# Performance work log

Hardware: AMD Instinct MI355X
Metric: run time of the kernel (lower is better)

Reference implementation:

```python
import jax, jax.numpy as jnp
import numpy as np

B, N_IN, N_E, N_I, N_OUT, T = 131072, 128, 128, 64, 128, 8


def setup_inputs() -> dict:
    key = jax.random.key(0)
    k0, k1, k2, k3, k4 = jax.random.split(key, 5)
    x = jax.random.normal(k0, (B, N_IN), dtype=jnp.float32)
    # nn.Linear weights are [out_features, in_features]; original init is uniform(0,1).
    # Scale by 1/fan_in to keep the relu recurrence numerically bounded over T steps.
    W_in2E = jax.random.uniform(k1, (N_E, N_IN), dtype=jnp.float32) / N_IN
    W_I2E = jax.random.uniform(k2, (N_E, N_I), dtype=jnp.float32) / N_I
    W_E2I = jax.random.uniform(k3, (N_I, N_E), dtype=jnp.float32) / N_E
    W_E2Out = jax.random.uniform(k4, (N_OUT, N_E), dtype=jnp.float32) / N_E
    return {"x": x, "W_in2E": W_in2E, "W_I2E": W_I2E, "W_E2I": W_E2I,
            "W_E2Out": W_E2Out, "num_timesteps": T}


def reference(x, W_in2E, W_I2E, W_E2I, W_E2Out, num_timesteps):
    # tau = 1 for every population, so each step: state = sum_proj W @ pre_activity,
    # activity = relu(state + bias) with bias = 0 (learn_bias defaults False).
    # Population order within a step: InputE -> H1E -> H1I -> OutE, so H1E uses
    # H1I's activity from the previous step (the recurrent carry).
    ff = x @ W_in2E.T                                  # [B, N_E], constant over steps

    def step(actI, _):
        actE = jax.nn.relu(ff + actI @ W_I2E.T)        # H1.E
        actI_new = jax.nn.relu(actE @ W_E2I.T)         # H1.I (uses current actE)
        out = jax.nn.relu(actE @ W_E2Out.T)            # Output.E
        return actI_new, out

    actI0 = jnp.zeros((x.shape[0], W_I2E.shape[1]), dtype=x.dtype)
    _, outs = jax.lax.scan(step, actI0, None, length=num_timesteps)
    return outs[-1]                                    # output_pop.activity after last step
```

## Files before the change

### kernel.cpp

```cpp
#include <hip/hip_runtime.h>
#include <hip/hip_bf16.h>


typedef __bf16 bf16x8_t __attribute__((ext_vector_type(8)));
typedef __bf16 bf16x4_t __attribute__((ext_vector_type(4)));
typedef float f32x4_t __attribute__((ext_vector_type(4)));

#define THREADS 512

#define S_WIN2E 272
#define S_WE2OUT 272
#define S_WI2E 144
#define S_WE2I 272
#define S_ACTE 272
#define S_ACTI 144

#define OFF_WIN2E 0
#define OFF_WE2OUT (OFF_WIN2E + 128 * S_WIN2E)
#define OFF_WI2E (OFF_WE2OUT + 128 * S_WE2OUT)
#define OFF_WE2I (OFF_WI2E + 128 * S_WI2E)
#define OFF_ACTE (OFF_WE2I + 64 * S_WE2I)
#define OFF_ACTI (OFF_ACTE + 8 * 16 * S_ACTE)
#define SMEM_TOTAL (OFF_ACTI + 8 * 16 * S_ACTI)

__device__ __forceinline__ f32x4_t mfma16(bf16x8_t a, bf16x8_t b, f32x4_t c) {
  return __builtin_amdgcn_mfma_f32_16x16x32_bf16(a, b, c, 0, 0, 0);
}

template <int ROWS, int COLS, int STRIDE_B>
__device__ __forceinline__ void stage_weight(const float* __restrict__ W,
                                             char* dst, int tid) {
  constexpr int TOTAL4 = ROWS * COLS / 4;
#pragma unroll
  for (int it = 0; it < TOTAL4 / THREADS; ++it) {
    int e = (it * THREADS + tid) * 4;
    int r = e / COLS;
    int c = e % COLS;
    float4 v = *reinterpret_cast<const float4*>(W + e);
    bf16x4_t h;
    h[0] = (__bf16)v.x; h[1] = (__bf16)v.y;
    h[2] = (__bf16)v.z; h[3] = (__bf16)v.w;
    *reinterpret_cast<bf16x4_t*>(dst + r * STRIDE_B + c * 2) = h;
  }
}

__global__ __launch_bounds__(THREADS, 2) void unet_fused(
    const float* __restrict__ x,
    const float* __restrict__ Win2E,
    const float* __restrict__ WI2E,
    const float* __restrict__ WE2I,
    const float* __restrict__ WE2Out,
    const int* __restrict__ Tptr,
    float* __restrict__ out) {
  extern __shared__ char smem[];
  const int tid = threadIdx.x;

  stage_weight<128, 128, S_WIN2E>(Win2E, smem + OFF_WIN2E, tid);
  stage_weight<128, 128, S_WE2OUT>(WE2Out, smem + OFF_WE2OUT, tid);
  stage_weight<128, 64, S_WI2E>(WI2E, smem + OFF_WI2E, tid);
  stage_weight<64, 128, S_WE2I>(WE2I, smem + OFF_WE2I, tid);
  __syncthreads();

  const int wid = tid >> 6;
  const int lane = tid & 63;
  const int m = lane & 15;
  const int kc = lane >> 4;
  const int T = *Tptr;

  char* actE = smem + OFF_ACTE + wid * (16 * S_ACTE);
  char* actI = smem + OFF_ACTI + wid * (16 * S_ACTI);

  bf16x8_t wi2e[8][2];
#pragma unroll
  for (int mt = 0; mt < 8; ++mt)
#pragma unroll
    for (int ks = 0; ks < 2; ++ks)
      wi2e[mt][ks] = *reinterpret_cast<const bf16x8_t*>(
          smem + OFF_WI2E + (mt * 16 + m) * S_WI2E + (ks * 32 + kc * 8) * 2);

  bf16x8_t we2i[4][4];
#pragma unroll
  for (int mt = 0; mt < 4; ++mt)
#pragma unroll
    for (int ks = 0; ks < 4; ++ks)
      we2i[mt][ks] = *reinterpret_cast<const bf16x8_t*>(
          smem + OFF_WE2I + (mt * 16 + m) * S_WE2I + (ks * 32 + kc * 8) * 2);

  const long row0 = ((long)blockIdx.x * 8 + wid) * 16;

  bf16x8_t xb[4];
#pragma unroll
  for (int ks = 0; ks < 4; ++ks) {
    const float* xp = x + (row0 + m) * 128 + ks * 32 + kc * 8;
    float4 v0 = *reinterpret_cast<const float4*>(xp);
    float4 v1 = *reinterpret_cast<const float4*>(xp + 4);
    bf16x8_t h;
    h[0] = (__bf16)v0.x; h[1] = (__bf16)v0.y; h[2] = (__bf16)v0.z; h[3] = (__bf16)v0.w;
    h[4] = (__bf16)v1.x; h[5] = (__bf16)v1.y; h[6] = (__bf16)v1.z; h[7] = (__bf16)v1.w;
    xb[ks] = h;
  }

  f32x4_t ff[8];
#pragma unroll
  for (int mt = 0; mt < 8; ++mt) ff[mt] = (f32x4_t){0.f, 0.f, 0.f, 0.f};
#pragma unroll
  for (int ks = 0; ks < 4; ++ks) {
#pragma unroll
    for (int mt = 0; mt < 8; ++mt) {
      bf16x8_t a = *reinterpret_cast<const bf16x8_t*>(
          smem + OFF_WIN2E + (mt * 16 + m) * S_WIN2E + (ks * 32 + kc * 8) * 2);
      ff[mt] = mfma16(a, xb[ks], ff[mt]);
    }
  }

  f32x4_t acc_e[8];
#pragma unroll
  for (int mt = 0; mt < 8; ++mt) acc_e[mt] = ff[mt];

  bf16x8_t eb[4];

  for (int t = 0;; ++t) {
#pragma unroll
    for (int mt = 0; mt < 8; ++mt) {
      bf16x4_t h;
#pragma unroll
      for (int j = 0; j < 4; ++j) h[j] = (__bf16)fmaxf(acc_e[mt][j], 0.f);
      *reinterpret_cast<bf16x4_t*>(actE + m * S_ACTE + (mt * 16 + kc * 4) * 2) = h;
    }
#pragma unroll
    for (int ks = 0; ks < 4; ++ks)
      eb[ks] = *reinterpret_cast<const bf16x8_t*>(
          actE + m * S_ACTE + (ks * 32 + kc * 8) * 2);
    if (t == T - 1) break;

    f32x4_t acc_i[4];
#pragma unroll
    for (int mt = 0; mt < 4; ++mt) acc_i[mt] = (f32x4_t){0.f, 0.f, 0.f, 0.f};
#pragma unroll
    for (int ks = 0; ks < 4; ++ks)
#pragma unroll
      for (int mt = 0; mt < 4; ++mt)
        acc_i[mt] = mfma16(we2i[mt][ks], eb[ks], acc_i[mt]);

#pragma unroll
    for (int mt = 0; mt < 4; ++mt) {
      bf16x4_t h;
#pragma unroll
      for (int j = 0; j < 4; ++j) h[j] = (__bf16)fmaxf(acc_i[mt][j], 0.f);
      *reinterpret_cast<bf16x4_t*>(actI + m * S_ACTI + (mt * 16 + kc * 4) * 2) = h;
    }
    bf16x8_t ib[2];
#pragma unroll
    for (int ks = 0; ks < 2; ++ks)
      ib[ks] = *reinterpret_cast<const bf16x8_t*>(
          actI + m * S_ACTI + (ks * 32 + kc * 8) * 2);

#pragma unroll
    for (int mt = 0; mt < 8; ++mt) acc_e[mt] = ff[mt];
#pragma unroll
    for (int ks = 0; ks < 2; ++ks)
#pragma unroll
      for (int mt = 0; mt < 8; ++mt)
        acc_e[mt] = mfma16(wi2e[mt][ks], ib[ks], acc_e[mt]);
  }

#pragma unroll
  for (int mt = 0; mt < 8; ++mt) {
    f32x4_t o = (f32x4_t){0.f, 0.f, 0.f, 0.f};
#pragma unroll
    for (int ks = 0; ks < 4; ++ks) {
      bf16x8_t a = *reinterpret_cast<const bf16x8_t*>(
          smem + OFF_WE2OUT + (mt * 16 + m) * S_WE2OUT + (ks * 32 + kc * 8) * 2);
      o = mfma16(a, eb[ks], o);
    }
    f32x4_t r;
#pragma unroll
    for (int j = 0; j < 4; ++j) r[j] = fmaxf(o[j], 0.f);
    *reinterpret_cast<f32x4_t*>(out + (row0 + m) * 128 + mt * 16 + kc * 4) = r;
  }
}

extern "C" void kernel_launch(void* const* d_in, const int* in_sizes, int n_in,
                              void* d_out, int out_size, void* d_ws,
                              size_t ws_size, hipStream_t stream) {
  const float* x = (const float*)d_in[0];
  const float* Win2E = (const float*)d_in[1];
  const float* WI2E = (const float*)d_in[2];
  const float* WE2I = (const float*)d_in[3];
  const float* WE2Out = (const float*)d_in[4];
  const int* Tptr = (const int*)d_in[5];
  float* out = (float*)d_out;
  (void)n_in; (void)out_size; (void)d_ws; (void)ws_size;

  const int B = in_sizes[0] / 128;
  (void)hipFuncSetAttribute(reinterpret_cast<const void*>(unet_fused),
                            hipFuncAttributeMaxDynamicSharedMemorySize,
                            SMEM_TOTAL);
  dim3 grid(B / 128), block(THREADS);
  unet_fused<<<grid, block, SMEM_TOTAL, stream>>>(x, Win2E, WI2E, WE2I, WE2Out,
                                                  Tptr, out);
}
```

Baseline: 61.95 us.

## Switch to 32x32 MFMA with register-resident activation transposes via permlane swap

Moves from 16x16x32 to 32x32x16 bf16 MFMA tiles, so each wave now handles 32 batch rows and the grid is halved. Weights are staged into shared memory already in per-lane fragment order, so loads need no padded strides. The per-step activation round trip through shared memory is replaced by in-register relu+pack and v_permlane32_swap to form the next B operands. Weight fragments are now reloaded from LDS on every step instead of being kept in registers, and register pressure from the 16-wide accumulators rises, which may hurt occupancy.

```diff
diff --git a/kernel.cpp b/kernel.cpp
--- a/kernel.cpp
+++ b/kernel.cpp
@@ -3,44 +3,75 @@
 
 
 typedef __bf16 bf16x8_t __attribute__((ext_vector_type(8)));
-typedef __bf16 bf16x4_t __attribute__((ext_vector_type(4)));
+typedef float f32x16_t __attribute__((ext_vector_type(16)));
 typedef float f32x4_t __attribute__((ext_vector_type(4)));
+typedef unsigned int uintx4_t __attribute__((ext_vector_type(4)));
 
 #define THREADS 512
 
-#define S_WIN2E 272
-#define S_WE2OUT 272
-#define S_WI2E 144
-#define S_WE2I 272
-#define S_ACTE 272
-#define S_ACTI 144
+#define OFF_WIN2E 0
+#define OFF_WI2E 32768
+#define OFF_WE2I 49152
+#define OFF_WE2OUT 65536
+#define SMEM_TOTAL 98304
 
-#define OFF_WIN2E 0
-#define OFF_WE2OUT (OFF_WIN2E + 128 * S_WIN2E)
-#define OFF_WI2E (OFF_WE2OUT + 128 * S_WE2OUT)
-#define OFF_WE2I (OFF_WI2E + 128 * S_WI2E)
-#define OFF_ACTE (OFF_WE2I + 64 * S_WE2I)
-#define OFF_ACTI (OFF_ACTE + 8 * 16 * S_ACTE)
-#define SMEM_TOTAL (OFF_ACTI + 8 * 16 * S_ACTI)
-
-__device__ __forceinline__ f32x4_t mfma16(bf16x8_t a, bf16x8_t b, f32x4_t c) {
-  return __builtin_amdgcn_mfma_f32_16x16x32_bf16(a, b, c, 0, 0, 0);
+__device__ __forceinline__ f32x16_t mfma32(bf16x8_t a, bf16x8_t b, f32x16_t c) {
+  return __builtin_amdgcn_mfma_f32_32x32x16_bf16(a, b, c, 0, 0, 0);
 }
 
-template <int ROWS, int COLS, int STRIDE_B>
-__device__ __forceinline__ void stage_weight(const float* __restrict__ W,
-                                             char* dst, int tid) {
-  constexpr int TOTAL4 = ROWS * COLS / 4;
+__device__ __forceinline__ void swap32(unsigned int& x, unsigned int& y) {
+  asm("v_permlane32_swap_b32 %0, %1" : "+v"(x), "+v"(y));
+}
+
+__device__ __forceinline__ unsigned int pack2_relu(float a, float b) {
+  unsigned short lo = __builtin_bit_cast(unsigned short, (__bf16)fmaxf(a, 0.f));
+  unsigned short hi = __builtin_bit_cast(unsigned short, (__bf16)fmaxf(b, 0.f));
+  return (unsigned int)lo | ((unsigned int)hi << 16);
+}
+
+__device__ __forceinline__ void tile_to_bfrags(const f32x16_t& t, bf16x8_t& fa,
+                                               bf16x8_t& fb) {
+  unsigned int P0 = pack2_relu(t[0], t[1]);
+  unsigned int P1 = pack2_relu(t[2], t[3]);
+  unsigned int P2 = pack2_relu(t[4], t[5]);
+  unsigned int P3 = pack2_relu(t[6], t[7]);
+  unsigned int P4 = pack2_relu(t[8], t[9]);
+  unsigned int P5 = pack2_relu(t[10], t[11]);
+  unsigned int P6 = pack2_relu(t[12], t[13]);
+  unsigned int P7 = pack2_relu(t[14], t[15]);
+  swap32(P0, P2);
+  swap32(P1, P3);
+  swap32(P4, P6);
+  swap32(P5, P7);
+  fa = __builtin_bit_cast(bf16x8_t, (uintx4_t){P0, P1, P2, P3});
+  fb = __builtin_bit_cast(bf16x8_t, (uintx4_t){P4, P5, P6, P7});
+}
+
+__device__ __forceinline__ bf16x8_t ldfrag(const char* smem, int off, int fi,
+                                           int lane) {
+  return *reinterpret_cast<const bf16x8_t*>(smem + off + (fi * 64 + lane) * 16);
+}
+
+template <int NMT, int NKS, int COLS>
+__device__ __forceinline__ void stage_frags(const float* __restrict__ W,
+                                            char* dst, int tid) {
+  constexpr int SLOTS = NMT * NKS * 64;
 #pragma unroll
-  for (int it = 0; it < TOTAL4 / THREADS; ++it) {
-    int e = (it * THREADS + tid) * 4;
-    int r = e / COLS;
-    int c = e % COLS;
-    float4 v = *reinterpret_cast<const float4*>(W + e);
-    bf16x4_t h;
-    h[0] = (__bf16)v.x; h[1] = (__bf16)v.y;
-    h[2] = (__bf16)v.z; h[3] = (__bf16)v.w;
-    *reinterpret_cast<bf16x4_t*>(dst + r * STRIDE_B + c * 2) = h;
+  for (int it = 0; it < SLOTS / THREADS; ++it) {
+    int slot = it * THREADS + tid;
+    int lane = slot & 63;
+    int fi = slot >> 6;
+    int mt = fi / NKS, ks = fi % NKS;
+    int cc = lane & 31, hh = lane >> 5;
+    const float* src = W + (mt * 32 + cc) * COLS + ks * 16 + hh * 8;
+    float4 v0 = *reinterpret_cast<const float4*>(src);
+    float4 v1 = *reinterpret_cast<const float4*>(src + 4);
+    bf16x8_t hv;
+    hv[0] = (__bf16)v0.x; hv[1] = (__bf16)v0.y;
+    hv[2] = (__bf16)v0.z; hv[3] = (__bf16)v0.w;
+    hv[4] = (__bf16)v1.x; hv[5] = (__bf16)v1.y;
+    hv[6] = (__bf16)v1.z; hv[7] = (__bf16)v1.w;
+    *reinterpret_cast<bf16x8_t*>(dst + slot * 16) = hv;
   }
 }
 
@@ -55,128 +86,94 @@
   extern __shared__ char smem[];
   const int tid = threadIdx.x;
 
-  stage_weight<128, 128, S_WIN2E>(Win2E, smem + OFF_WIN2E, tid);
-  stage_weight<128, 128, S_WE2OUT>(WE2Out, smem + OFF_WE2OUT, tid);
-  stage_weight<128, 64, S_WI2E>(WI2E, smem + OFF_WI2E, tid);
-  stage_weight<64, 128, S_WE2I>(WE2I, smem + OFF_WE2I, tid);
+  stage_frags<4, 8, 128>(Win2E, smem + OFF_WIN2E, tid);
+  stage_frags<4, 4, 64>(WI2E, smem + OFF_WI2E, tid);
+  stage_frags<2, 8, 128>(WE2I, smem + OFF_WE2I, tid);
+  stage_frags<4, 8, 128>(WE2Out, smem + OFF_WE2OUT, tid);
   __syncthreads();
 
-  const int wid = tid >> 6;
-  const int lane = tid & 63;
-  const int m = lane & 15;
-  const int kc = lane >> 4;
+  const int wid = tid >> 6, lane = tid & 63;
+  const int c = lane & 31, h = lane >> 5;
   const int T = *Tptr;
+  const long row0 = ((long)blockIdx.x * 8 + wid) * 32;
+  const f32x16_t Z = {};
 
-  char* actE = smem + OFF_ACTE + wid * (16 * S_ACTE);
-  char* actI = smem + OFF_ACTI + wid * (16 * S_ACTI);
+  bf16x8_t xb[8];
+#pragma unroll
+  for (int ks = 0; ks < 8; ++ks) {
+    const float* xp = x + (row0 + c) * 128 + ks * 16 + h * 8;
+    float4 v0 = *reinterpret_cast<const float4*>(xp);
+    float4 v1 = *reinterpret_cast<const float4*>(xp + 4);
+    bf16x8_t hv;
+    hv[0] = (__bf16)v0.x; hv[1] = (__bf16)v0.y;
+    hv[2] = (__bf16)v0.z; hv[3] = (__bf16)v0.w;
+    hv[4] = (__bf16)v1.x; hv[5] = (__bf16)v1.y;
+    hv[6] = (__bf16)v1.z; hv[7] = (__bf16)v1.w;
+    xb[ks] = hv;
+  }
 
-  bf16x8_t wi2e[8][2];
-#pragma unroll
-  for (int mt = 0; mt < 8; ++mt)
-#pragma unroll
-    for (int ks = 0; ks < 2; ++ks)
-      wi2e[mt][ks] = *reinterpret_cast<const bf16x8_t*>(
-          smem + OFF_WI2E + (mt * 16 + m) * S_WI2E + (ks * 32 + kc * 8) * 2);
-
-  bf16x8_t we2i[4][4];
+  f32x16_t ff[4];
 #pragma unroll
   for (int mt = 0; mt < 4; ++mt)
+    ff[mt] = mfma32(ldfrag(smem, OFF_WIN2E, mt * 8 + 0, lane), xb[0], Z);
 #pragma unroll
-    for (int ks = 0; ks < 4; ++ks)
-      we2i[mt][ks] = *reinterpret_cast<const bf16x8_t*>(
-          smem + OFF_WE2I + (mt * 16 + m) * S_WE2I + (ks * 32 + kc * 8) * 2);
+  for (int ks = 1; ks < 8; ++ks)
+#pragma unroll
+    for (int mt = 0; mt < 4; ++mt)
+      ff[mt] = mfma32(ldfrag(smem, OFF_WIN2E, mt * 8 + ks, lane), xb[ks], ff[mt]);
 
-  const long row0 = ((long)blockIdx.x * 8 + wid) * 16;
+  f32x16_t acc_e[4];
+#pragma unroll
+  for (int mt = 0; mt < 4; ++mt) acc_e[mt] = ff[mt];
 
-  bf16x8_t xb[4];
-#pragma unroll
-  for (int ks = 0; ks < 4; ++ks) {
-    const float* xp = x + (row0 + m) * 128 + ks * 32 + kc * 8;
-    float4 v0 = *reinterpret_cast<const float4*>(xp);
-    float4 v1 = *reinterpret_cast<const float4*>(xp + 4);
-    bf16x8_t h;
-    h[0] = (__bf16)v0.x; h[1] = (__bf16)v0.y; h[2] = (__bf16)v0.z; h[3] = (__bf16)v0.w;
-    h[4] = (__bf16)v1.x; h[5] = (__bf16)v1.y; h[6] = (__bf16)v1.z; h[7] = (__bf16)v1.w;
-    xb[ks] = h;
-  }
-
-  f32x4_t ff[8];
-#pragma unroll
-  for (int mt = 0; mt < 8; ++mt) ff[mt] = (f32x4_t){0.f, 0.f, 0.f, 0.f};
-#pragma unroll
-  for (int ks = 0; ks < 4; ++ks) {
-#pragma unroll
-    for (int mt = 0; mt < 8; ++mt) {
-      bf16x8_t a = *reinterpret_cast<const bf16x8_t*>(
-          smem + OFF_WIN2E + (mt * 16 + m) * S_WIN2E + (ks * 32 + kc * 8) * 2);
-      ff[mt] = mfma16(a, xb[ks], ff[mt]);
-    }
-  }
-
-  f32x4_t acc_e[8];
-#pragma unroll
-  for (int mt = 0; mt < 8; ++mt) acc_e[mt] = ff[mt];
-
-  bf16x8_t eb[4];
-
+  bf16x8_t eb[8];
   for (int t = 0;; ++t) {
 #pragma unroll
-    for (int mt = 0; mt < 8; ++mt) {
-      bf16x4_t h;
-#pragma unroll
-      for (int j = 0; j < 4; ++j) h[j] = (__bf16)fmaxf(acc_e[mt][j], 0.f);
-      *reinterpret_cast<bf16x4_t*>(actE + m * S_ACTE + (mt * 16 + kc * 4) * 2) = h;
-    }
-#pragma unroll
-    for (int ks = 0; ks < 4; ++ks)
-      eb[ks] = *reinterpret_cast<const bf16x8_t*>(
-          actE + m * S_ACTE + (ks * 32 + kc * 8) * 2);
+    for (int mt = 0; mt < 4; ++mt)
+      tile_to_bfrags(acc_e[mt], eb[2 * mt], eb[2 * mt + 1]);
     if (t == T - 1) break;
 
-    f32x4_t acc_i[4];
+    f32x16_t acc_i[2];
 #pragma unroll
-    for (int mt = 0; mt < 4; ++mt) acc_i[mt] = (f32x4_t){0.f, 0.f, 0.f, 0.f};
+    for (int mt = 0; mt < 2; ++mt)
+      acc_i[mt] = mfma32(ldfrag(smem, OFF_WE2I, mt * 8 + 0, lane), eb[0], Z);
 #pragma unroll
-    for (int ks = 0; ks < 4; ++ks)
+    for (int ks = 1; ks < 8; ++ks)
+#pragma unroll
+      for (int mt = 0; mt < 2; ++mt)
+        acc_i[mt] =
+            mfma32(ldfrag(smem, OFF_WE2I, mt * 8 + ks, lane), eb[ks], acc_i[mt]);
+
+    bf16x8_t ib[4];
+#pragma unroll
+    for (int mt = 0; mt < 2; ++mt)
+      tile_to_bfrags(acc_i[mt], ib[2 * mt], ib[2 * mt + 1]);
+
+#pragma unroll
+    for (int mt = 0; mt < 4; ++mt)
+      acc_e[mt] = mfma32(ldfrag(smem, OFF_WI2E, mt * 4 + 0, lane), ib[0], ff[mt]);
+#pragma unroll
+    for (int ks = 1; ks < 4; ++ks)
 #pragma unroll
       for (int mt = 0; mt < 4; ++mt)
-        acc_i[mt] = mfma16(we2i[mt][ks], eb[ks], acc_i[mt]);
-
-#pragma unroll
-    for (int mt = 0; mt < 4; ++mt) {
-      bf16x4_t h;
-#pragma unroll
-      for (int j = 0; j < 4; ++j) h[j] = (__bf16)fmaxf(acc_i[mt][j], 0.f);
-      *reinterpret_cast<bf16x4_t*>(actI + m * S_ACTI + (mt * 16 + kc * 4) * 2) = h;
-    }
-    bf16x8_t ib[2];
-#pragma unroll
-    for (int ks = 0; ks < 2; ++ks)
-      ib[ks] = *reinterpret_cast<const bf16x8_t*>(
-          actI + m * S_ACTI + (ks * 32 + kc * 8) * 2);
-
-#pragma unroll
-    for (int mt = 0; mt < 8; ++mt) acc_e[mt] = ff[mt];
-#pragma unroll
-    for (int ks = 0; ks < 2; ++ks)
-#pragma unroll
-      for (int mt = 0; mt < 8; ++mt)
-        acc_e[mt] = mfma16(wi2e[mt][ks], ib[ks], acc_e[mt]);
+        acc_e[mt] =
+            mfma32(ldfrag(smem, OFF_WI2E, mt * 4 + ks, lane), ib[ks], acc_e[mt]);
   }
 
 #pragma unroll
-  for (int mt = 0; mt < 8; ++mt) {
-    f32x4_t o = (f32x4_t){0.f, 0.f, 0.f, 0.f};
+  for (int mt = 0; mt < 4; ++mt) {
+    f32x16_t o = mfma32(ldfrag(smem, OFF_WE2OUT, mt * 8 + 0, lane), eb[0], Z);
 #pragma unroll
-    for (int ks = 0; ks < 4; ++ks) {
-      bf16x8_t a = *reinterpret_cast<const bf16x8_t*>(
-          smem + OFF_WE2OUT + (mt * 16 + m) * S_WE2OUT + (ks * 32 + kc * 8) * 2);
-      o = mfma16(a, eb[ks], o);
+    for (int ks = 1; ks < 8; ++ks)
+      o = mfma32(ldfrag(smem, OFF_WE2OUT, mt * 8 + ks, lane), eb[ks], o);
+#pragma unroll
+    for (int q = 0; q < 4; ++q) {
+      f32x4_t r;
+#pragma unroll
+      for (int s = 0; s < 4; ++s) r[s] = fmaxf(o[4 * q + s], 0.f);
+      *reinterpret_cast<f32x4_t*>(out + (row0 + c) * 128 + mt * 32 + q * 8 +
+                                  4 * h) = r;
     }
-    f32x4_t r;
-#pragma unroll
-    for (int j = 0; j < 4; ++j) r[j] = fmaxf(o[j], 0.f);
-    *reinterpret_cast<f32x4_t*>(out + (row0 + m) * 128 + mt * 16 + kc * 4) = r;
   }
 }
 
@@ -196,7 +193,7 @@
   (void)hipFuncSetAttribute(reinterpret_cast<const void*>(unet_fused),
                             hipFuncAttributeMaxDynamicSharedMemorySize,
                             SMEM_TOTAL);
-  dim3 grid(B / 128), block(THREADS);
+  dim3 grid(B / 256), block(THREADS);
   unet_fused<<<grid, block, SMEM_TOTAL, stream>>>(x, Win2E, WI2E, WE2I, WE2Out,
                                                   Tptr, out);
 }
```

Measured after the change: 68.52 us. 1.11x slower.

## Drop shared memory; remap activations in registers via permlane swaps

Applied to the files above, without the earlier changes.

Removes all LDS staging. Weight fragments are now read directly from global memory (through the cache) and converted to bf16 per wave. The activation round trip through shared memory between MFMA stages is replaced by in-register v_permlane32/16 swaps that reshape accumulator layouts into B-operand fragments. Block size drops to 256 threads with twice the blocks, and x loads are issued early. This trades the LDS traffic and the large shared-memory footprint, which limited occupancy, for redundant global weight reads by every wave plus permlane ALU work.

```diff
diff --git a/kernel.cpp b/kernel.cpp
--- a/kernel.cpp
+++ b/kernel.cpp
@@ -3,45 +3,55 @@
 
 
 typedef __bf16 bf16x8_t __attribute__((ext_vector_type(8)));
-typedef __bf16 bf16x4_t __attribute__((ext_vector_type(4)));
 typedef float f32x4_t __attribute__((ext_vector_type(4)));
+typedef unsigned int uintx4_t __attribute__((ext_vector_type(4)));
 
-#define THREADS 512
-
-#define S_WIN2E 272
-#define S_WE2OUT 272
-#define S_WI2E 144
-#define S_WE2I 272
-#define S_ACTE 272
-#define S_ACTI 144
-
-#define OFF_WIN2E 0
-#define OFF_WE2OUT (OFF_WIN2E + 128 * S_WIN2E)
-#define OFF_WI2E (OFF_WE2OUT + 128 * S_WE2OUT)
-#define OFF_WE2I (OFF_WI2E + 128 * S_WI2E)
-#define OFF_ACTE (OFF_WE2I + 64 * S_WE2I)
-#define OFF_ACTI (OFF_ACTE + 8 * 16 * S_ACTE)
-#define SMEM_TOTAL (OFF_ACTI + 8 * 16 * S_ACTI)
+#define THREADS 256
 
 __device__ __forceinline__ f32x4_t mfma16(bf16x8_t a, bf16x8_t b, f32x4_t c) {
   return __builtin_amdgcn_mfma_f32_16x16x32_bf16(a, b, c, 0, 0, 0);
 }
 
-template <int ROWS, int COLS, int STRIDE_B>
-__device__ __forceinline__ void stage_weight(const float* __restrict__ W,
-                                             char* dst, int tid) {
-  constexpr int TOTAL4 = ROWS * COLS / 4;
-#pragma unroll
-  for (int it = 0; it < TOTAL4 / THREADS; ++it) {
-    int e = (it * THREADS + tid) * 4;
-    int r = e / COLS;
-    int c = e % COLS;
-    float4 v = *reinterpret_cast<const float4*>(W + e);
-    bf16x4_t h;
-    h[0] = (__bf16)v.x; h[1] = (__bf16)v.y;
-    h[2] = (__bf16)v.z; h[3] = (__bf16)v.w;
-    *reinterpret_cast<bf16x4_t*>(dst + r * STRIDE_B + c * 2) = h;
-  }
+__device__ __forceinline__ void swap32(unsigned int& x, unsigned int& y) {
+  asm("v_permlane32_swap_b32 %0, %1" : "+v"(x), "+v"(y));
+}
+__device__ __forceinline__ void swap16(unsigned int& x, unsigned int& y) {
+  asm("v_permlane16_swap_b32 %0, %1" : "+v"(x), "+v"(y));
+}
+
+__device__ __forceinline__ unsigned int pack2_relu(float a, float b) {
+  unsigned short lo = __builtin_bit_cast(unsigned short, (__bf16)fmaxf(a, 0.f));
+  unsigned short hi = __builtin_bit_cast(unsigned short, (__bf16)fmaxf(b, 0.f));
+  return (unsigned int)lo | ((unsigned int)hi << 16);
+}
+
+__device__ __forceinline__ bf16x8_t remap2(const f32x4_t& t0,
+                                           const f32x4_t& t1) {
+  unsigned int A0 = pack2_relu(t0[0], t0[1]);
+  unsigned int A1 = pack2_relu(t0[2], t0[3]);
+  unsigned int B0 = pack2_relu(t1[0], t1[1]);
+  unsigned int B1 = pack2_relu(t1[2], t1[3]);
+  swap32(A0, B0);
+  swap16(A0, B0);
+  swap32(A1, B1);
+  swap16(A1, B1);
+  return __builtin_bit_cast(bf16x8_t, (uintx4_t){A0, A1, B0, B1});
+}
+
+__device__ __forceinline__ bf16x8_t cvt8(float4 v0, float4 v1) {
+  bf16x8_t h;
+  h[0] = (__bf16)v0.x; h[1] = (__bf16)v0.y;
+  h[2] = (__bf16)v0.z; h[3] = (__bf16)v0.w;
+  h[4] = (__bf16)v1.x; h[5] = (__bf16)v1.y;
+  h[6] = (__bf16)v1.z; h[7] = (__bf16)v1.w;
+  return h;
+}
+
+__device__ __forceinline__ bf16x8_t gfrag(const float* __restrict__ W,
+                                          int off) {
+  float4 v0 = *reinterpret_cast<const float4*>(W + off);
+  float4 v1 = *reinterpret_cast<const float4*>(W + off + 4);
+  return cvt8(v0, v1);
 }
 
 __global__ __launch_bounds__(THREADS, 2) void unet_fused(
@@ -52,131 +62,85 @@
     const float* __restrict__ WE2Out,
     const int* __restrict__ Tptr,
     float* __restrict__ out) {
-  extern __shared__ char smem[];
   const int tid = threadIdx.x;
+  const int wid = tid >> 6, lane = tid & 63;
+  const int c = lane & 15, q = lane >> 4;
+  const int T = *Tptr;
+  const long row0 = ((long)blockIdx.x * 4 + wid) * 16;
+  const f32x4_t Z = {};
 
-  stage_weight<128, 128, S_WIN2E>(Win2E, smem + OFF_WIN2E, tid);
-  stage_weight<128, 128, S_WE2OUT>(WE2Out, smem + OFF_WE2OUT, tid);
-  stage_weight<128, 64, S_WI2E>(WI2E, smem + OFF_WI2E, tid);
-  stage_weight<64, 128, S_WE2I>(WE2I, smem + OFF_WE2I, tid);
-  __syncthreads();
-
-  const int wid = tid >> 6;
-  const int lane = tid & 63;
-  const int m = lane & 15;
-  const int kc = lane >> 4;
-  const int T = *Tptr;
-
-  char* actE = smem + OFF_ACTE + wid * (16 * S_ACTE);
-  char* actI = smem + OFF_ACTI + wid * (16 * S_ACTI);
+  const float* xrow = x + (row0 + c) * 128 + q * 8;
+  float4 xv[8];
+#pragma unroll
+  for (int s = 0; s < 4; ++s) {
+    xv[2 * s] = *reinterpret_cast<const float4*>(xrow + s * 32);
+    xv[2 * s + 1] = *reinterpret_cast<const float4*>(xrow + s * 32 + 4);
+  }
 
   bf16x8_t wi2e[8][2];
 #pragma unroll
   for (int mt = 0; mt < 8; ++mt)
 #pragma unroll
-    for (int ks = 0; ks < 2; ++ks)
-      wi2e[mt][ks] = *reinterpret_cast<const bf16x8_t*>(
-          smem + OFF_WI2E + (mt * 16 + m) * S_WI2E + (ks * 32 + kc * 8) * 2);
-
+    for (int s = 0; s < 2; ++s)
+      wi2e[mt][s] = gfrag(WI2E, (mt * 16 + c) * 64 + s * 32 + q * 8);
   bf16x8_t we2i[4][4];
 #pragma unroll
   for (int mt = 0; mt < 4; ++mt)
 #pragma unroll
-    for (int ks = 0; ks < 4; ++ks)
-      we2i[mt][ks] = *reinterpret_cast<const bf16x8_t*>(
-          smem + OFF_WE2I + (mt * 16 + m) * S_WE2I + (ks * 32 + kc * 8) * 2);
-
-  const long row0 = ((long)blockIdx.x * 8 + wid) * 16;
+    for (int s = 0; s < 4; ++s)
+      we2i[mt][s] = gfrag(WE2I, (mt * 16 + c) * 128 + s * 32 + q * 8);
 
   bf16x8_t xb[4];
 #pragma unroll
-  for (int ks = 0; ks < 4; ++ks) {
-    const float* xp = x + (row0 + m) * 128 + ks * 32 + kc * 8;
-    float4 v0 = *reinterpret_cast<const float4*>(xp);
-    float4 v1 = *reinterpret_cast<const float4*>(xp + 4);
-    bf16x8_t h;
-    h[0] = (__bf16)v0.x; h[1] = (__bf16)v0.y; h[2] = (__bf16)v0.z; h[3] = (__bf16)v0.w;
-    h[4] = (__bf16)v1.x; h[5] = (__bf16)v1.y; h[6] = (__bf16)v1.z; h[7] = (__bf16)v1.w;
-    xb[ks] = h;
-  }
+  for (int s = 0; s < 4; ++s) xb[s] = cvt8(xv[2 * s], xv[2 * s + 1]);
 
   f32x4_t ff[8];
 #pragma unroll
-  for (int mt = 0; mt < 8; ++mt) ff[mt] = (f32x4_t){0.f, 0.f, 0.f, 0.f};
+  for (int mt = 0; mt < 8; ++mt)
+    ff[mt] = mfma16(gfrag(Win2E, (mt * 16 + c) * 128 + q * 8), xb[0], Z);
 #pragma unroll
-  for (int ks = 0; ks < 4; ++ks) {
+  for (int s = 1; s < 4; ++s)
 #pragma unroll
-    for (int mt = 0; mt < 8; ++mt) {
-      bf16x8_t a = *reinterpret_cast<const bf16x8_t*>(
-          smem + OFF_WIN2E + (mt * 16 + m) * S_WIN2E + (ks * 32 + kc * 8) * 2);
-      ff[mt] = mfma16(a, xb[ks], ff[mt]);
-    }
-  }
+    for (int mt = 0; mt < 8; ++mt)
+      ff[mt] = mfma16(gfrag(Win2E, (mt * 16 + c) * 128 + s * 32 + q * 8),
+                      xb[s], ff[mt]);
 
   f32x4_t acc_e[8];
 #pragma unroll
   for (int mt = 0; mt < 8; ++mt) acc_e[mt] = ff[mt];
 
-  bf16x8_t eb[4];
-
-  for (int t = 0;; ++t) {
+  for (int t = 0; t < T - 1; ++t) {
+    f32x4_t acc_i[4];
 #pragma unroll
-    for (int mt = 0; mt < 8; ++mt) {
-      bf16x4_t h;
+    for (int s = 0; s < 4; ++s) {
+      bf16x8_t ebs = remap2(acc_e[2 * s], acc_e[2 * s + 1]);
 #pragma unroll
-      for (int j = 0; j < 4; ++j) h[j] = (__bf16)fmaxf(acc_e[mt][j], 0.f);
-      *reinterpret_cast<bf16x4_t*>(actE + m * S_ACTE + (mt * 16 + kc * 4) * 2) = h;
+      for (int mt = 0; mt < 4; ++mt)
+        acc_i[mt] = mfma16(we2i[mt][s], ebs, s == 0 ? Z : acc_i[mt]);
     }
 #pragma unroll
-    for (int ks = 0; ks < 4; ++ks)
-      eb[ks] = *reinterpret_cast<const bf16x8_t*>(
-          actE + m * S_ACTE + (ks * 32 + kc * 8) * 2);
-    if (t == T - 1) break;
-
-    f32x4_t acc_i[4];
-#pragma unroll
-    for (int mt = 0; mt < 4; ++mt) acc_i[mt] = (f32x4_t){0.f, 0.f, 0.f, 0.f};
-#pragma unroll
-    for (int ks = 0; ks < 4; ++ks)
-#pragma unroll
-      for (int mt = 0; mt < 4; ++mt)
-        acc_i[mt] = mfma16(we2i[mt][ks], eb[ks], acc_i[mt]);
-
-#pragma unroll
-    for (int mt = 0; mt < 4; ++mt) {
-      bf16x4_t h;
-#pragma unroll
-      for (int j = 0; j < 4; ++j) h[j] = (__bf16)fmaxf(acc_i[mt][j], 0.f);
-      *reinterpret_cast<bf16x4_t*>(actI + m * S_ACTI + (mt * 16 + kc * 4) * 2) = h;
-    }
-    bf16x8_t ib[2];
-#pragma unroll
-    for (int ks = 0; ks < 2; ++ks)
-      ib[ks] = *reinterpret_cast<const bf16x8_t*>(
-          actI + m * S_ACTI + (ks * 32 + kc * 8) * 2);
-
-#pragma unroll
-    for (int mt = 0; mt < 8; ++mt) acc_e[mt] = ff[mt];
-#pragma unroll
-    for (int ks = 0; ks < 2; ++ks)
+    for (int s = 0; s < 2; ++s) {
+      bf16x8_t ibs = remap2(acc_i[2 * s], acc_i[2 * s + 1]);
 #pragma unroll
       for (int mt = 0; mt < 8; ++mt)
-        acc_e[mt] = mfma16(wi2e[mt][ks], ib[ks], acc_e[mt]);
+        acc_e[mt] = mfma16(wi2e[mt][s], ibs, s == 0 ? ff[mt] : acc_e[mt]);
+    }
   }
 
+  bf16x8_t eb[4];
+#pragma unroll
+  for (int s = 0; s < 4; ++s)
+    eb[s] = remap2(acc_e[2 * s], acc_e[2 * s + 1]);
 #pragma unroll
   for (int mt = 0; mt < 8; ++mt) {
-    f32x4_t o = (f32x4_t){0.f, 0.f, 0.f, 0.f};
+    f32x4_t o = mfma16(gfrag(WE2Out, (mt * 16 + c) * 128 + q * 8), eb[0], Z);
 #pragma unroll
-    for (int ks = 0; ks < 4; ++ks) {
-      bf16x8_t a = *reinterpret_cast<const bf16x8_t*>(
-          smem + OFF_WE2OUT + (mt * 16 + m) * S_WE2OUT + (ks * 32 + kc * 8) * 2);
-      o = mfma16(a, eb[ks], o);
-    }
+    for (int s = 1; s < 4; ++s)
+      o = mfma16(gfrag(WE2Out, (mt * 16 + c) * 128 + s * 32 + q * 8), eb[s], o);
     f32x4_t r;
 #pragma unroll
     for (int j = 0; j < 4; ++j) r[j] = fmaxf(o[j], 0.f);
-    *reinterpret_cast<f32x4_t*>(out + (row0 + m) * 128 + mt * 16 + kc * 4) = r;
+    *reinterpret_cast<f32x4_t*>(out + (row0 + c) * 128 + mt * 16 + q * 4) = r;
   }
 }
 
@@ -193,10 +157,7 @@
   (void)n_in; (void)out_size; (void)d_ws; (void)ws_size;
 
   const int B = in_sizes[0] / 128;
-  (void)hipFuncSetAttribute(reinterpret_cast<const void*>(unet_fused),
-                            hipFuncAttributeMaxDynamicSharedMemorySize,
-                            SMEM_TOTAL);
-  dim3 grid(B / 128), block(THREADS);
-  unet_fused<<<grid, block, SMEM_TOTAL, stream>>>(x, Win2E, WI2E, WE2I, WE2Out,
-                                                  Tptr, out);
+  dim3 grid(B / 64), block(THREADS);
+  unet_fused<<<grid, block, 0, stream>>>(x, Win2E, WI2E, WE2I, WE2Out, Tptr,
+                                         out);
 }
```

Result: slower. 189.4 us (+205.8%).
